# Kernel optimization log

Measured on AMD Instinct MI355X. Metric: run time of the kernel, lower is better.

Reference implementation:

```python
import jax, jax.numpy as jnp
import numpy as np

B, V, T, C, H = 2, 4, 512, 768, 12
HD = C // H          # head dim = 64
QD = H * HD          # q_dim = 768
EPS_RMS = 1e-5
EPS_LN = 1e-6


def rotate_two(x):
    # interleaved pair rotation: (x0,x1,x2,x3,...) -> (-x1,x0,-x3,x2,...)
    return jnp.reshape(jnp.concatenate((-1.0 * x[..., 1::2, None], x[..., ::2, None]), axis=-1), x.shape)


def layer_norm(x, scale, bias=None):
    mu = jnp.mean(x, axis=-1, keepdims=True)
    xc = x - mu
    var = jnp.mean(xc * xc, axis=-1, keepdims=True)
    y = xc * jax.lax.rsqrt(var + EPS_LN) * scale
    return y + bias if bias is not None else y


def rms_norm(x, alpha):
    # alpha has shape [H, HD], broadcasts over leading dims
    mag = jnp.sqrt(jnp.mean(x.astype(jnp.float32) ** 2, axis=-1, keepdims=True) + EPS_RMS).astype(x.dtype)
    return alpha * x / mag


def apply_rope(x, sc):
    # x: [B,V,T,H,HD], sc: [T,HD,2]
    cos = sc[None, None, :, None, :, 0]
    sin = sc[None, None, :, None, :, 1]
    return x * cos + rotate_two(x) * sin


def seg_attention(q, k, v, seg):
    # q,k,v: [N,S,H,D] fp32; seg: [N,S] int. bf16 qkv as in the original flash-attn call.
    qb, kb, vb = (t.astype(jnp.bfloat16) for t in (q, k, v))
    scale = 1.0 / np.sqrt(q.shape[-1]).astype(np.float32)
    scores = jnp.einsum('bqhd,bkhd->bhqk', qb, kb, preferred_element_type=jnp.float32) * scale
    same = (seg[:, None, :, None] == seg[:, None, None, :])  # [N,1,S,S]
    scores = jnp.where(same, scores, jnp.float32(-1e30))
    attn = jax.nn.softmax(scores, axis=-1)
    out = jnp.einsum('bhqk,bkhd->bqhd', attn.astype(jnp.bfloat16), vb, preferred_element_type=jnp.float32)
    return out.astype(q.dtype)


def setup_inputs() -> dict:
    key = jax.random.key(0)
    ks = jax.random.split(key, 16)
    x = jax.random.normal(ks[0], (B, V, T, C), dtype=jnp.float32)
    patch_ids = jnp.sort(jax.random.randint(ks[1], (B, T), 0, 8), axis=-1).astype(jnp.int32)
    # standard RoPE table, pairs repeated to match rotate_two's interleaved layout
    inv_freq = 1.0 / (10000.0 ** (np.arange(0, HD, 2, dtype=np.float32) / HD))
    ang = np.arange(T, dtype=np.float32)[:, None] * inv_freq[None, :]       # [T, HD/2]
    cos = np.repeat(np.cos(ang), 2, axis=-1)                                 # [T, HD]
    sin = np.repeat(np.sin(ang), 2, axis=-1)
    sincos_rope = jnp.asarray(np.stack([cos, sin], axis=-1), dtype=jnp.float32)  # [T,HD,2]
    s = 0.02
    return {
        'x': x,
        'patch_ids': patch_ids,
        'sincos_rope': sincos_rope,
        'ln1_scale': jnp.ones((C,), jnp.float32),
        'w_qkv': jax.random.normal(ks[2], (C, 6 * QD), jnp.float32) * s,
        'rms_q_alpha': jnp.ones((H, HD), jnp.float32),
        'rms_k_alpha': jnp.ones((H, HD), jnp.float32),
        'rms_qs_alpha': jnp.ones((H, HD), jnp.float32),
        'rms_ks_alpha': jnp.ones((H, HD), jnp.float32),
        'w_out': jax.random.normal(ks[3], (2 * QD, C), jnp.float32) * s,
        'b_out': jax.random.normal(ks[4], (C,), jnp.float32) * 1e-6,
        'ls1_alpha': jnp.full((C,), 0.01, jnp.float32),
        'ln2_scale': jnp.ones((C,), jnp.float32),
        'ln2_bias': jnp.zeros((C,), jnp.float32),
        'w_mlp1': jax.random.normal(ks[5], (C, 4 * C), jnp.float32) * s,
        'b_mlp1': jax.random.normal(ks[6], (4 * C,), jnp.float32) * 1e-6,
        'w_mlp2': jax.random.normal(ks[7], (4 * C, C), jnp.float32) * s,
        'b_mlp2': jax.random.normal(ks[8], (C,), jnp.float32) * 1e-6,
        'ls2_alpha': jnp.full((C,), 0.01, jnp.float32),
    }


def reference(x, patch_ids, sincos_rope, ln1_scale, w_qkv, rms_q_alpha, rms_k_alpha,
              rms_qs_alpha, rms_ks_alpha, w_out, b_out, ls1_alpha, ln2_scale, ln2_bias,
              w_mlp1, b_mlp1, w_mlp2, b_mlp2, ls2_alpha):
    x_in = layer_norm(x, ln1_scale)                       # [B,V,T,C]
    qkv = x_in @ w_qkv                                    # [B,V,T,6*QD]
    q, k, v, qs, ks, vs = [p.reshape(B, V, T, H, HD) for p in jnp.split(qkv, 6, axis=-1)]
    q = rms_norm(q, rms_q_alpha)
    k = rms_norm(k, rms_k_alpha)
    qs = rms_norm(qs, rms_qs_alpha)
    ks = rms_norm(ks, rms_ks_alpha)
    q, k = apply_rope(q, sincos_rope), apply_rope(k, sincos_rope)
    qs, ks = apply_rope(qs, sincos_rope), apply_rope(ks, sincos_rope)
    # global attention: views concatenated along sequence -> [B, V*T, H, HD]
    qg, kg, vg = (t.reshape(B, V * T, H, HD) for t in (q, k, v))
    seg_g = jnp.tile(patch_ids, (1, V))                   # [B, V*T]
    xg = seg_attention(qg, kg, vg, seg_g).reshape(B, V, T, QD)
    # self-view attention: views concatenated along batch -> [V*B, T, H, HD]
    qs_, ks_, vs_ = (t.transpose(1, 0, 2, 3, 4).reshape(V * B, T, H, HD) for t in (qs, ks, vs))
    seg_s = jnp.tile(patch_ids[None], (V, 1, 1)).reshape(V * B, T)
    xs = seg_attention(qs_, ks_, vs_, seg_s).reshape(V, B, T, QD).transpose(1, 0, 2, 3)
    x0 = jnp.concatenate((xg, xs), axis=-1) @ w_out + b_out
    x0 = ls1_alpha * x0 + x                               # LayerScale + residual
    x1 = jax.nn.gelu(layer_norm(x0, ln2_scale, ln2_bias))
    x1 = jax.nn.gelu(x1 @ w_mlp1 + b_mlp1) @ w_mlp2 + b_mlp2
    return ls2_alpha * x1 + x0
```

## Files before the change

### kernel.cpp

```cpp
#include <hip/hip_runtime.h>

#define DEVI __device__ __forceinline__

typedef __attribute__((ext_vector_type(8))) short short8;
typedef __attribute__((ext_vector_type(4))) float f32x4;
typedef unsigned short u16;

DEVI u16 f2bf(float f){
  unsigned int u = __float_as_uint(f);
  unsigned int r = (u + 0x7FFFu + ((u>>16)&1u)) >> 16;
  return (u16)r;
}
DEVI float bf2f(u16 h){ return __uint_as_float(((unsigned int)h)<<16); }

DEVI unsigned int cvt_pk_bf16(float a, float b){
  unsigned int r;
  asm("v_cvt_pk_bf16_f32 %0, %1, %2" : "=v"(r) : "v"(a), "v"(b));
  return r;
}

DEVI float gelu_f(float x){
  float x3 = x*x*x;
  float t = tanhf(0.7978845608028654f*(x + 0.044715f*x3));
  return 0.5f*x*(1.0f + t);
}

DEVI void async_cp16(const void* g, void* l){
  __builtin_amdgcn_global_load_lds(
      (const __attribute__((address_space(1))) unsigned int*)g,
      (__attribute__((address_space(3))) unsigned int*)l, 16, 0, 0);
}

DEVI void wtrans_body(const float* __restrict__ w, u16* __restrict__ wt,
                      int K, int N, int bx, int by, int tid){
  __shared__ float tile[32][33];
  int tn = bx*32, tk = by*32;
  int r = tid>>3, c4 = (tid&7)*4;
  float4 vv = *(const float4*)&w[(size_t)(tk+r)*N + tn + c4];
  tile[r][c4+0]=vv.x; tile[r][c4+1]=vv.y; tile[r][c4+2]=vv.z; tile[r][c4+3]=vv.w;
  __syncthreads();
  u16 o[4];
  #pragma unroll
  for (int j=0;j<4;j++) o[j] = f2bf(tile[c4+j][r]);
  unsigned long long pk = (unsigned long long)o[0] | ((unsigned long long)o[1]<<16)
                        | ((unsigned long long)o[2]<<32) | ((unsigned long long)o[3]<<48);
  *(unsigned long long*)&wt[(size_t)(tn+r)*K + tk + c4] = pk;
}

DEVI void ln1_body(const float* __restrict__ x, const float* __restrict__ sc,
                   u16* __restrict__ xin, int row, int tid){
  __shared__ float ls0[4], ls1_[4];
  const float* xr = x + (size_t)row*768;
  float v[3]; float s=0.f, ss=0.f;
  #pragma unroll
  for (int i=0;i<3;i++){ v[i]=xr[tid+i*256]; s+=v[i]; ss+=v[i]*v[i]; }
  #pragma unroll
  for (int m=1;m<=32;m<<=1){ s += __shfl_xor(s,m,64); ss += __shfl_xor(ss,m,64); }
  int w = tid>>6;
  if ((tid&63)==0){ ls0[w]=s; ls1_[w]=ss; }
  __syncthreads();
  s = ls0[0]+ls0[1]+ls0[2]+ls0[3]; ss = ls1_[0]+ls1_[1]+ls1_[2]+ls1_[3];
  float mu = s*(1.f/768.f);
  float var = ss*(1.f/768.f) - mu*mu;
  float inv = rsqrtf(var + 1e-6f);
  #pragma unroll
  for (int i=0;i<3;i++){ int c=tid+i*256; xin[(size_t)row*768+c] = f2bf((v[i]-mu)*inv*sc[c]); }
}

__global__ __launch_bounds__(256) void prep_k(
    const float* __restrict__ w0, u16* __restrict__ o0,
    const float* __restrict__ w1, u16* __restrict__ o1,
    const float* __restrict__ w2, u16* __restrict__ o2,
    const float* __restrict__ w3, u16* __restrict__ o3,
    const float* __restrict__ x,  const float* __restrict__ ln1s,
    u16* __restrict__ xin)
{
  int bid = blockIdx.x, tid = threadIdx.x;
  if (bid < 3456){            wtrans_body(w0,o0, 768,4608, bid%144, bid/144, tid); }
  else if (bid < 4608){ int b=bid-3456; wtrans_body(w1,o1,1536, 768, b%24,  b/24,  tid); }
  else if (bid < 6912){ int b=bid-4608; wtrans_body(w2,o2, 768,3072, b%96,  b/96,  tid); }
  else if (bid < 9216){ int b=bid-6912; wtrans_body(w3,o3,3072, 768, b%24,  b/24,  tid); }
  else                { ln1_body(x, ln1s, xin, bid-9216, tid); }
}

template<int EPI, int SPLITK, int K, int N>
__global__ __launch_bounds__(256) void gemm_k(
    const u16* __restrict__ A, const u16* __restrict__ Bt,
    u16* __restrict__ Cb, const float* __restrict__ bias)
{
  constexpr int M = 4096;
  constexpr int Ksub = K/SPLITK;
  __shared__ __align__(16) u16 Al[128*64];
  __shared__ __align__(16) u16 Bl[128*64];
  const int tid = threadIdx.x, w = tid>>6, l = tid&63;
  int bx, by, kc;
  if (SPLITK>1){
    int id = blockIdx.x;
    int xcd = id&7, j = id>>3;
    bx = j%6; int rr = (j/6)&3; kc = j/24;
    by = xcd*4 + rr;
  } else { bx = blockIdx.x; by = blockIdx.y; kc = 0; }
  const int m0 = by*128, n0 = bx*128;
  const int kbase = kc*Ksub;
  const int wr = (w>>1)*64, wc = (w&1)*64;
  f32x4 acc[4][4];
  #pragma unroll
  for (int i=0;i<4;i++)
    #pragma unroll
    for (int j2=0;j2<4;j2++){ f32x4 z={0.f,0.f,0.f,0.f}; acc[i][j2]=z; }
  const int srow0 = tid>>3, sc16 = tid&7;
  #pragma unroll
  for (int k0=0; k0<Ksub; k0+=64){
    __syncthreads();
    #pragma unroll
    for (int it=0; it<4; ++it){
      int row = it*32 + srow0;
      int sc = sc16 ^ (row&7);
      async_cp16(A  + (size_t)(m0+row)*K + kbase + k0 + sc*8, &Al[(it*256+tid)*8]);
      async_cp16(Bt + (size_t)(n0+row)*K + kbase + k0 + sc*8, &Bl[(it*256+tid)*8]);
    }
    __syncthreads();
    #pragma unroll
    for (int ks=0; ks<2; ++ks){
      short8 af[4], bfr[4];
      #pragma unroll
      for (int mi=0;mi<4;++mi){
        int row = wr + mi*16 + (l&15);
        int boff = row*128 + (((l>>4)*16 + ks*64) ^ ((row&7)<<4));
        af[mi] = *(const short8*)((const char*)&Al[0] + boff);
      }
      #pragma unroll
      for (int ni=0;ni<4;++ni){
        int row = wc + ni*16 + (l&15);
        int boff = row*128 + (((l>>4)*16 + ks*64) ^ ((row&7)<<4));
        bfr[ni] = *(const short8*)((const char*)&Bl[0] + boff);
      }
      #pragma unroll
      for (int mi=0;mi<4;++mi)
        #pragma unroll
        for (int ni=0;ni<4;++ni)
          acc[mi][ni] = __builtin_amdgcn_mfma_f32_16x16x32_bf16(af[mi], bfr[ni], acc[mi][ni], 0,0,0);
    }
  }
  #pragma unroll
  for (int mi=0;mi<4;++mi){
    int rb = m0 + wr + mi*16 + ((l>>4)<<2);
    #pragma unroll
    for (int ni=0;ni<4;++ni){
      int col = n0 + wc + ni*16 + (l&15);
      #pragma unroll
      for (int r=0;r<4;r++){
        int row = rb + r;
        float v = acc[mi][ni][r];
        if (EPI==0)      Cb[((size_t)kc*M + row)*N + col] = f2bf(v);
        else if (EPI==2) Cb[(size_t)row*N+col] = f2bf(gelu_f(v + bias[col]));
        else             Cb[(size_t)row*N+col] = f2bf(v);
      }
    }
  }
}

__global__ __launch_bounds__(256) void redln_k(
    const u16* __restrict__ P, const float* __restrict__ bias,
    const float* __restrict__ lsc, const float* __restrict__ resid,
    const float* __restrict__ ln2sc, const float* __restrict__ ln2bi,
    float* __restrict__ x0, u16* __restrict__ x1)
{
  const size_t MN = 4096ull*768;
  int row = blockIdx.x, tid = threadIdx.x;
  float v[3]; float s=0.f, ss=0.f;
  #pragma unroll
  for (int i=0;i<3;i++){
    int c = tid + i*256;
    size_t idx = (size_t)row*768 + c;
    float acc = bf2f(P[idx]) + bf2f(P[MN+idx]) + bf2f(P[2*MN+idx]) + bf2f(P[3*MN+idx]);
    float y = lsc[c]*(acc + bias[c]) + resid[idx];
    x0[idx] = y;
    v[i] = y; s += y; ss += y*y;
  }
  #pragma unroll
  for (int m=1;m<=32;m<<=1){ s += __shfl_xor(s,m,64); ss += __shfl_xor(ss,m,64); }
  __shared__ float ls0[4], ls1_[4];
  int w = tid>>6;
  if ((tid&63)==0){ ls0[w]=s; ls1_[w]=ss; }
  __syncthreads();
  s = ls0[0]+ls0[1]+ls0[2]+ls0[3]; ss = ls1_[0]+ls1_[1]+ls1_[2]+ls1_[3];
  float mu = s*(1.f/768.f);
  float var = ss*(1.f/768.f) - mu*mu;
  float inv = rsqrtf(var + 1e-6f);
  #pragma unroll
  for (int i=0;i<3;i++){
    int c = tid + i*256;
    float y = (v[i]-mu)*inv*ln2sc[c] + ln2bi[c];
    x1[(size_t)row*768 + c] = f2bf(gelu_f(y));
  }
}

__global__ __launch_bounds__(256) void red_k(
    const u16* __restrict__ P, const float* __restrict__ bias,
    const float* __restrict__ lsc, const float* __restrict__ resid,
    float* __restrict__ out)
{
  const size_t MN = 4096ull*768;
  size_t i = ((size_t)blockIdx.x*256 + threadIdx.x)*4;
  int c = (int)(i % 768);
  ushort4 a0 = *(const ushort4*)&P[i];
  ushort4 a1 = *(const ushort4*)&P[MN+i];
  ushort4 a2 = *(const ushort4*)&P[2*MN+i];
  ushort4 a3 = *(const ushort4*)&P[3*MN+i];
  float4 bi = *(const float4*)&bias[c];
  float4 ls = *(const float4*)&lsc[c];
  float4 rs = *(const float4*)&resid[i];
  float4 o;
  o.x = ls.x*(bf2f(a0.x)+bf2f(a1.x)+bf2f(a2.x)+bf2f(a3.x) + bi.x) + rs.x;
  o.y = ls.y*(bf2f(a0.y)+bf2f(a1.y)+bf2f(a2.y)+bf2f(a3.y) + bi.y) + rs.y;
  o.z = ls.z*(bf2f(a0.z)+bf2f(a1.z)+bf2f(a2.z)+bf2f(a3.z) + bi.z) + rs.z;
  o.w = ls.w*(bf2f(a0.w)+bf2f(a1.w)+bf2f(a2.w)+bf2f(a3.w) + bi.w) + rs.w;
  *(float4*)&out[i] = o;
}

__global__ __launch_bounds__(256) void postproc2_k(
  const u16* __restrict__ qkv, const float* __restrict__ sincos,
  const float* __restrict__ aq, const float* __restrict__ ak,
  const float* __restrict__ aqs, const float* __restrict__ aks,
  u16* __restrict__ qg, u16* __restrict__ kg, u16* __restrict__ vg,
  u16* __restrict__ qsg, u16* __restrict__ ksg, u16* __restrict__ vsg)
{
  __shared__ u16 vt[2][64*66];
  const int bid = blockIdx.x;
  const int b = bid/384; int r0 = bid - b*384;
  const int v = r0/96;   int r1 = r0 - v*96;
  const int t6 = r1/12;  const int h = r1 - t6*12;
  const int T0 = t6*64;
  const int tid = threadIdx.x, w = tid>>6, l = tid&63;
  const int tq = l>>4, dq = l&15;
  const int m0 = b*2048 + v*512;
  const size_t gQbase = ((size_t)(b*12) + h)*2048 + v*512;
  const size_t sQbase = ((size_t)((v*2+b)*12) + h)*512;

  #pragma unroll
  for (int qi=0; qi<4; ++qi){
    const int tt = (qi<2) ? qi : qi+1;
    const float* al = (qi==0)?aq:(qi==1)?ak:(qi==2)?aqs:aks;
    float4 alv = *(const float4*)&al[h*64 + dq*4];
    u16* dst = (qi==0)?qg:(qi==1)?kg:(qi==2)?qsg:ksg;
    const size_t obase = (qi<2) ? gQbase : sQbase;
    #pragma unroll
    for (int it=0; it<4; ++it){
      const int t = T0 + w*16 + it*4 + tq;
      const u16* src = &qkv[(size_t)(m0+t)*4608 + tt*768 + h*64 + dq*4];
      ushort2 u01 = *(const ushort2*)src;
      ushort2 u23 = *(const ushort2*)(src+2);
      float x0=bf2f(u01.x), x1=bf2f(u01.y), x2=bf2f(u23.x), x3=bf2f(u23.y);
      float ss = x0*x0+x1*x1+x2*x2+x3*x3;
      #pragma unroll
      for (int mm=1;mm<=8;mm<<=1) ss += __shfl_xor(ss,mm,64);
      float rinv = rsqrtf(ss*(1.f/64.f) + 1e-5f);
      x0 *= alv.x*rinv; x1 *= alv.y*rinv; x2 *= alv.z*rinv; x3 *= alv.w*rinv;
      float4 cs01 = *(const float4*)&sincos[(size_t)(t*64 + dq*4)*2];
      float4 cs23 = *(const float4*)&sincos[(size_t)(t*64 + dq*4)*2 + 4];
      float y0 = x0*cs01.x - x1*cs01.y;
      float y1 = x1*cs01.z + x0*cs01.w;
      float y2 = x2*cs23.x - x3*cs23.y;
      float y3 = x3*cs23.z + x2*cs23.w;
      unsigned int lo = cvt_pk_bf16(y0, y1);
      unsigned int hi = cvt_pk_bf16(y2, y3);
      unsigned int* po = (unsigned int*)&dst[(obase + t)*64 + dq*4];
      po[0] = lo; po[1] = hi;
    }
  }

  #pragma unroll
  for (int vi=0; vi<2; ++vi){
    const int tt = (vi==0) ? 2 : 5;
    #pragma unroll
    for (int it=0; it<4; ++it){
      const int t = T0 + w*16 + it*4 + tq;
      const int tl = w*16 + it*4 + tq;
      const u16* src = &qkv[(size_t)(m0+t)*4608 + tt*768 + h*64 + dq*4];
      ushort2 u01 = *(const ushort2*)src;
      ushort2 u23 = *(const ushort2*)(src+2);
      unsigned int* pl = (unsigned int*)&vt[vi][tl*66 + dq*4];
      pl[0] = (unsigned int)u01.x | ((unsigned int)u01.y<<16);
      pl[1] = (unsigned int)u23.x | ((unsigned int)u23.y<<16);
    }
  }
  __syncthreads();
  {
    const size_t vgb = (((size_t)(b*12) + h)*64)*2048 + v*512 + T0 + l;
    #pragma unroll
    for (int i=0;i<16;++i){
      int d = w*16 + i;
      vg[vgb + (size_t)d*2048] = vt[0][l*66 + d];
    }
    const size_t vsb = (((size_t)((v*2+b)*12) + h)*64)*512 + T0 + l;
    #pragma unroll
    for (int i=0;i<16;++i){
      int d = w*16 + i;
      vsg[vsb + (size_t)d*512] = vt[1][l*66 + d];
    }
  }
}

__global__ __launch_bounds__(256) void attn7_k(
  const u16* __restrict__ Qg, const u16* __restrict__ Kg, const u16* __restrict__ Vtg,
  const u16* __restrict__ Qs, const u16* __restrict__ Ks, const u16* __restrict__ Vts,
  u16* __restrict__ Out, const int* __restrict__ pids)
{
  __shared__ __align__(16) u16 Kl[64*64];
  __shared__ __align__(16) u16 Vl[64*64];
  __shared__ __align__(16) u16 Pl[4][16*64];
  __shared__ unsigned long long amask_s;
  const int gid = blockIdx.x;
  const int xcd = gid & 7, idx = gid >> 3;
  const int lid = (idx < 96) ? xcd*96 + idx : 768 + xcd*96 + (idx - 96);
  const int tid = threadIdx.x, w = tid>>6, l = tid&63;
  const u16 *Q, *K, *Vt; const int* prow;
  int L, seq, h, qb, orow0, ocol;
  if (lid < 768){
    seq = lid/384; int rem2 = lid - seq*384; h = rem2>>5; qb = rem2&31;
    Q=Qg; K=Kg; Vt=Vtg; L=2048;
    prow = pids + seq*512; orow0 = seq*2048; ocol = h*64;
  } else {
    int g2 = lid - 768; seq = g2/96; int rem2 = g2 - seq*96; h = rem2>>3; qb = rem2&7;
    Q=Qs; K=Ks; Vt=Vts; L=512;
    prow = pids + (seq&1)*512; orow0 = (seq&1)*2048 + (seq>>1)*512; ocol = 768 + h*64;
  }
  const size_t base = ((size_t)(seq*12) + h)*(size_t)L*64;
  const int q0 = qb*64, tq0 = q0 & 511;
  short8 qf[2];
  const int qrow = q0 + w*16 + (l&15);
  #pragma unroll
  for (int s=0;s<2;s++) qf[s] = *(const short8*)&Q[base + (size_t)qrow*64 + s*32 + (l>>4)*8];
  const int qlo = prow[tq0], qhi = prow[tq0+63];
  int sq[4];
  #pragma unroll
  for (int r=0;r<4;r++) sq[r] = prow[tq0 + w*16 + (l>>4)*4 + r];
  float lsum[4]; f32x4 ao[4];
  #pragma unroll
  for (int r=0;r<4;r++) lsum[r]=0.f;
  #pragma unroll
  for (int d=0;d<4;d++){ f32x4 z={0.f,0.f,0.f,0.f}; ao[d]=z; }
  const int nk = L/64;
  bool act = false;
  if (tid < 64 && tid < nk){
    int tk0 = (tid*64)&511;
    act = (prow[tk0+63] >= qlo) && (prow[tk0] <= qhi);
  }
  unsigned long long bm = __ballot(act);
  if (tid==0) amask_s = bm;
  __syncthreads();
  unsigned long long rem = amask_s;
  int t = (int)(__ffsll((unsigned long long)rem)-1); rem &= rem-1;
  const int srow0 = tid>>3, sc16 = tid&7;
  while (true){
    const int k0 = t*64;
    __syncthreads();
    #pragma unroll
    for (int it=0; it<2; ++it){
      int row = it*32 + srow0;
      int sc = sc16 ^ (row&7);
      async_cp16(&K[base + (size_t)(k0+row)*64 + sc*8],        &Kl[(it*256+tid)*8]);
      async_cp16(&Vt[base + (size_t)row*(size_t)L + k0 + sc*8], &Vl[(it*256+tid)*8]);
    }
    __syncthreads();
    const int tk0 = (t*64) & 511;
    int skv[4];
    #pragma unroll
    for (int kb=0;kb<4;kb++) skv[kb] = prow[tk0 + kb*16 + (l&15)];
    f32x4 s4[4];
    #pragma unroll
    for (int kb=0;kb<4;kb++){
      const int krow = kb*16 + (l&15);
      f32x4 a = {0.f,0.f,0.f,0.f};
      #pragma unroll
      for (int s=0;s<2;s++){
        int boff = krow*128 + ((s*64 + (l>>4)*16) ^ ((krow&7)<<4));
        short8 kf = *(const short8*)((const char*)&Kl[0] + boff);
        a = __builtin_amdgcn_mfma_f32_16x16x32_bf16(qf[s], kf, a, 0,0,0);
      }
      s4[kb] = a;
    }
    #pragma unroll
    for (int kb=0;kb<4;kb++){
      float p0 = (skv[kb] == sq[0]) ? __expf(s4[kb][0]*0.125f) : 0.f;
      float p1 = (skv[kb] == sq[1]) ? __expf(s4[kb][1]*0.125f) : 0.f;
      float p2 = (skv[kb] == sq[2]) ? __expf(s4[kb][2]*0.125f) : 0.f;
      float p3 = (skv[kb] == sq[3]) ? __expf(s4[kb][3]*0.125f) : 0.f;
      lsum[0]+=p0; lsum[1]+=p1; lsum[2]+=p2; lsum[3]+=p3;
      unsigned int u01 = cvt_pk_bf16(p0, p1);
      unsigned int u23 = cvt_pk_bf16(p2, p3);
      int prw0 = (l>>4)*4;
      Pl[w][(prw0+0)*64 + (((kb*32 + (l&15)*2) ^ (((prw0+0)&7)<<4))>>1)] = (u16)u01;
      Pl[w][(prw0+1)*64 + (((kb*32 + (l&15)*2) ^ (((prw0+1)&7)<<4))>>1)] = (u16)(u01>>16);
      Pl[w][(prw0+2)*64 + (((kb*32 + (l&15)*2) ^ (((prw0+2)&7)<<4))>>1)] = (u16)u23;
      Pl[w][(prw0+3)*64 + (((kb*32 + (l&15)*2) ^ (((prw0+3)&7)<<4))>>1)] = (u16)(u23>>16);
    }
    short8 pa[2];
    #pragma unroll
    for (int s=0;s<2;s++)
      pa[s] = *(const short8*)&Pl[w][(l&15)*64 + (((s*64 + (l>>4)*16) ^ (((l&15)&7)<<4))>>1)];
    #pragma unroll
    for (int d=0;d<4;d++){
      const int vrow = d*16 + (l&15);
      #pragma unroll
      for (int s=0;s<2;s++){
        int boff = vrow*128 + ((s*64 + (l>>4)*16) ^ ((vrow&7)<<4));
        short8 vf = *(const short8*)((const char*)&Vl[0] + boff);
        ao[d] = __builtin_amdgcn_mfma_f32_16x16x32_bf16(pa[s], vf, ao[d], 0,0,0);
      }
    }
    if (!rem) break;
    t = (int)(__ffsll((unsigned long long)rem)-1); rem &= rem-1;
  }
  #pragma unroll
  for (int r=0;r<4;r++){
    #pragma unroll
    for (int m=1;m<=8;m<<=1) lsum[r] += __shfl_xor(lsum[r], m, 64);
    lsum[r] = 1.0f / lsum[r];
  }
  #pragma unroll
  for (int d=0;d<4;d++){
    unsigned int u01 = cvt_pk_bf16(ao[d][0]*lsum[0], ao[d][1]*lsum[1]);
    unsigned int u23 = cvt_pk_bf16(ao[d][2]*lsum[2], ao[d][3]*lsum[3]);
    int prw0 = (l>>4)*4, col = d*16 + (l&15);
    Pl[w][(prw0+0)*64 + col] = (u16)u01;
    Pl[w][(prw0+1)*64 + col] = (u16)(u01>>16);
    Pl[w][(prw0+2)*64 + col] = (u16)u23;
    Pl[w][(prw0+3)*64 + col] = (u16)(u23>>16);
  }
  __builtin_amdgcn_s_waitcnt(0);
  {
    int r16 = l&15, cchunk = (l>>4)*16;
    uint4 v0 = *(const uint4*)&Pl[w][r16*64 + cchunk];
    uint4 v1 = *(const uint4*)&Pl[w][r16*64 + cchunk + 8];
    size_t orow = (size_t)(orow0 + q0 + w*16 + r16)*1536 + ocol + cchunk;
    *(uint4*)&Out[orow]     = v0;
    *(uint4*)&Out[orow + 8] = v1;
  }
}

extern "C" void kernel_launch(void* const* d_in, const int* in_sizes, int n_in,
                              void* d_out, int out_size, void* d_ws, size_t ws_size,
                              hipStream_t stream) {
  const float* x      = (const float*)d_in[0];
  const int*   patch  = (const int*)d_in[1];
  const float* sincos = (const float*)d_in[2];
  const float* ln1s   = (const float*)d_in[3];
  const float* wqkv   = (const float*)d_in[4];
  const float* aq     = (const float*)d_in[5];
  const float* ak     = (const float*)d_in[6];
  const float* aqs    = (const float*)d_in[7];
  const float* aks    = (const float*)d_in[8];
  const float* wout   = (const float*)d_in[9];
  const float* bout   = (const float*)d_in[10];
  const float* ls1    = (const float*)d_in[11];
  const float* ln2s   = (const float*)d_in[12];
  const float* ln2b   = (const float*)d_in[13];
  const float* wm1    = (const float*)d_in[14];
  const float* bm1    = (const float*)d_in[15];
  const float* wm2    = (const float*)d_in[16];
  const float* bm2    = (const float*)d_in[17];
  const float* ls2    = (const float*)d_in[18];
  float* out = (float*)d_out;

  char* ws = (char*)d_ws;
  size_t off = 0;
  auto alloc = [&](size_t bytes)->void*{ void* p = ws + off; off += (bytes + 255) & ~(size_t)255; return p; };
  u16*  wqkvT = (u16*)alloc(4608ull*768*2);
  u16*  woutT = (u16*)alloc(768ull*1536*2);
  u16*  wm1T  = (u16*)alloc(3072ull*768*2);
  u16*  wm2T  = (u16*)alloc(768ull*3072*2);
  u16*  xin   = (u16*)alloc(4096ull*768*2);
  u16*  qkvb  = (u16*)alloc(4096ull*4608*2);
  u16*  qg    = (u16*)alloc(3145728ull*2);
  u16*  kg    = (u16*)alloc(3145728ull*2);
  u16*  vg    = (u16*)alloc(3145728ull*2);
  u16*  qsg   = (u16*)alloc(3145728ull*2);
  u16*  ksg   = (u16*)alloc(3145728ull*2);
  u16*  vsg   = (u16*)alloc(3145728ull*2);
  u16*  cat   = (u16*)alloc(4096ull*1536*2);
  float* x0   = (float*)alloc(4096ull*768*4);
  u16*  x1    = (u16*)alloc(4096ull*768*2);
  u16*  hbuf  = (u16*)alloc(4096ull*3072*2);
  u16*  P     = qkvb;

  dim3 b256(256);
  prep_k<<<13312,b256,0,stream>>>(wqkv,wqkvT, wout,woutT, wm1,wm1T, wm2,wm2T, x, ln1s, xin);
  gemm_k<3,1,768,4608><<<dim3(36,32),b256,0,stream>>>(xin, wqkvT, qkvb, nullptr);
  postproc2_k<<<768,b256,0,stream>>>(qkvb, sincos, aq, ak, aqs, aks, qg,kg,vg,qsg,ksg,vsg);
  attn7_k<<<1536,b256,0,stream>>>(qg,kg,vg, qsg,ksg,vsg, cat, patch);
  gemm_k<0,4,1536,768><<<768,b256,0,stream>>>(cat, woutT, P, nullptr);
  redln_k<<<4096,b256,0,stream>>>(P, bout, ls1, x, ln2s, ln2b, x0, x1);
  gemm_k<2,1,768,3072><<<dim3(24,32),b256,0,stream>>>(x1, wm1T, hbuf, bm1);
  gemm_k<0,4,3072,768><<<768,b256,0,stream>>>(hbuf, wm2T, P, nullptr);
  red_k<<<3072,b256,0,stream>>>(P, bm2, ls2, x0, out);
}
```

Baseline: 188.6 us.

## Double-buffer K/V tiles in attention kernel to prefetch the next active tile

The attention kernel now keeps two LDS buffers for K and V. It issues the async global-to-LDS copy of the next active key tile before computing on the current one, instead of loading and then waiting at the top of every iteration. This is meant to hide global load latency behind the MFMA and softmax work and to drop one barrier per iteration. The cost is twice the K/V LDS footprint, which may lower occupancy per CU.

```diff
diff --git a/kernel.cpp b/kernel.cpp
--- a/kernel.cpp
+++ b/kernel.cpp
@@ -302,13 +302,13 @@
   }
 }
 
-__global__ __launch_bounds__(256) void attn7_k(
+__global__ __launch_bounds__(256) void attn8_k(
   const u16* __restrict__ Qg, const u16* __restrict__ Kg, const u16* __restrict__ Vtg,
   const u16* __restrict__ Qs, const u16* __restrict__ Ks, const u16* __restrict__ Vts,
   u16* __restrict__ Out, const int* __restrict__ pids)
 {
-  __shared__ __align__(16) u16 Kl[64*64];
-  __shared__ __align__(16) u16 Vl[64*64];
+  __shared__ __align__(16) u16 Kl[2][64*64];
+  __shared__ __align__(16) u16 Vl[2][64*64];
   __shared__ __align__(16) u16 Pl[4][16*64];
   __shared__ unsigned long long amask_s;
   const int gid = blockIdx.x;
@@ -353,17 +353,31 @@
   unsigned long long rem = amask_s;
   int t = (int)(__ffsll((unsigned long long)rem)-1); rem &= rem-1;
   const int srow0 = tid>>3, sc16 = tid&7;
-  while (true){
-    const int k0 = t*64;
-    __syncthreads();
+  {
+    int k0 = t*64;
     #pragma unroll
     for (int it=0; it<2; ++it){
       int row = it*32 + srow0;
       int sc = sc16 ^ (row&7);
-      async_cp16(&K[base + (size_t)(k0+row)*64 + sc*8],        &Kl[(it*256+tid)*8]);
-      async_cp16(&Vt[base + (size_t)row*(size_t)L + k0 + sc*8], &Vl[(it*256+tid)*8]);
-    }
-    __syncthreads();
+      async_cp16(&K[base + (size_t)(k0+row)*64 + sc*8],         &Kl[0][(it*256+tid)*8]);
+      async_cp16(&Vt[base + (size_t)row*(size_t)L + k0 + sc*8], &Vl[0][(it*256+tid)*8]);
+    }
+  }
+  __syncthreads();
+  int cur = 0;
+  while (true){
+    int tn = rem ? (int)(__ffsll((unsigned long long)rem)-1) : -1;
+    if (tn >= 0){
+      rem &= rem-1;
+      int k0n = tn*64;
+      #pragma unroll
+      for (int it=0; it<2; ++it){
+        int row = it*32 + srow0;
+        int sc = sc16 ^ (row&7);
+        async_cp16(&K[base + (size_t)(k0n+row)*64 + sc*8],         &Kl[cur^1][(it*256+tid)*8]);
+        async_cp16(&Vt[base + (size_t)row*(size_t)L + k0n + sc*8], &Vl[cur^1][(it*256+tid)*8]);
+      }
+    }
     const int tk0 = (t*64) & 511;
     int skv[4];
     #pragma unroll
@@ -376,7 +390,7 @@
       #pragma unroll
       for (int s=0;s<2;s++){
         int boff = krow*128 + ((s*64 + (l>>4)*16) ^ ((krow&7)<<4));
-        short8 kf = *(const short8*)((const char*)&Kl[0] + boff);
+        short8 kf = *(const short8*)((const char*)&Kl[cur][0] + boff);
         a = __builtin_amdgcn_mfma_f32_16x16x32_bf16(qf[s], kf, a, 0,0,0);
       }
       s4[kb] = a;
@@ -406,12 +420,13 @@
       #pragma unroll
       for (int s=0;s<2;s++){
         int boff = vrow*128 + ((s*64 + (l>>4)*16) ^ ((vrow&7)<<4));
-        short8 vf = *(const short8*)((const char*)&Vl[0] + boff);
+        short8 vf = *(const short8*)((const char*)&Vl[cur][0] + boff);
         ao[d] = __builtin_amdgcn_mfma_f32_16x16x32_bf16(pa[s], vf, ao[d], 0,0,0);
       }
     }
-    if (!rem) break;
-    t = (int)(__ffsll((unsigned long long)rem)-1); rem &= rem-1;
+    if (tn < 0) break;
+    __syncthreads();
+    cur ^= 1; t = tn;
   }
   #pragma unroll
   for (int r=0;r<4;r++){
@@ -489,7 +504,7 @@
   prep_k<<<13312,b256,0,stream>>>(wqkv,wqkvT, wout,woutT, wm1,wm1T, wm2,wm2T, x, ln1s, xin);
   gemm_k<3,1,768,4608><<<dim3(36,32),b256,0,stream>>>(xin, wqkvT, qkvb, nullptr);
   postproc2_k<<<768,b256,0,stream>>>(qkvb, sincos, aq, ak, aqs, aks, qg,kg,vg,qsg,ksg,vsg);
-  attn7_k<<<1536,b256,0,stream>>>(qg,kg,vg, qsg,ksg,vsg, cat, patch);
+  attn8_k<<<1536,b256,0,stream>>>(qg,kg,vg, qsg,ksg,vsg, cat, patch);
   gemm_k<0,4,1536,768><<<768,b256,0,stream>>>(cat, woutT, P, nullptr);
   redln_k<<<4096,b256,0,stream>>>(P, bout, ls1, x, ln2s, ln2b, x0, x1);
   gemm_k<2,1,768,3072><<<dim3(24,32),b256,0,stream>>>(x1, wm1T, hbuf, bm1);
```

New measurement: 191.8 us. About the same (+1.7%).
